# Performance work log

Measured on AMD Instinct MI355X. Metric: run time of the kernel, lower is better.

Reference implementation:

```python
import jax, jax.numpy as jnp
import numpy as np

FEATURE_MAPS = [8, 4, 2, 1]
BOXES_PER_LOC = [4, 6, 6, 4]
IMAGE_SIZE = 128
DECODED_SIZE = 64
Z_WHAT = 64
CHANNELS = [64, 256, 128, 64, 32, 16, 3]  # conv-transpose pyramid 1x1 -> 64x64
BATCH = 4
EMPTY_CONST = -1000.0
N_LOC = sum(f * f for f in FEATURE_MAPS)            # 85
N_BOX = sum(f * f * b for f, b in zip(FEATURE_MAPS, BOXES_PER_LOC))  # 380


def _recon_indices():
    # Decoder.reconstruction_indices: expand per-location latents to per-box.
    idx, last = [], 0
    for fm, bpl in zip(FEATURE_MAPS, BOXES_PER_LOC):
        for i in range(fm * fm):
            idx.append(np.full(bpl, last + i, dtype=np.int32))
        last += fm * fm
    return np.concatenate(idx)


def setup_inputs() -> dict:
    key = jax.random.key(0)
    ks = jax.random.split(key, 16)
    inp = {
        'z_what': jax.random.normal(ks[0], (BATCH, N_LOC, Z_WHAT), jnp.float32),
        'z_where': jax.random.uniform(ks[1], (BATCH, N_BOX, 4), jnp.float32),
        'z_present': jax.random.randint(ks[2], (BATCH, N_BOX, 1), 0, 2).astype(jnp.int32),
        'z_depth': jax.random.normal(ks[3], (BATCH, N_LOC, 1), jnp.float32),
    }
    for i, (cin, cout) in enumerate(zip(CHANNELS[:-1], CHANNELS[1:])):
        inp[f'w{i}'] = jax.random.normal(ks[4 + i], (2, 2, cin, cout), jnp.float32) / np.sqrt(4.0 * cin)
        inp[f'b{i}'] = jnp.zeros((cout,), jnp.float32)
    return inp


def _what_decoder(z_flat, params):
    # (N, Z) -> (N, 3, 64, 64): stack of stride-2 kernel-2 conv transposes.
    x = z_flat[:, :, None, None]
    n = len(params)
    for i, (w, b) in enumerate(params):
        x = jax.lax.conv_transpose(x, w, strides=(2, 2), padding='VALID',
                                   dimension_numbers=('NCHW', 'HWIO', 'NCHW'))
        x = x + b[None, :, None, None]
        x = jax.nn.sigmoid(x) if i == n - 1 else jax.nn.relu(x)
    return x


def _sample_bilinear(img, px, py):
    # img (3, D, D); px/py (S,) pixel coords along cols/rows; zero outside.
    D = DECODED_SIZE
    x0 = jnp.floor(px)
    y0 = jnp.floor(py)
    wx = px - x0
    wy = py - y0

    def gather(yi, xi):
        vy = (yi >= 0) & (yi <= D - 1)
        vx = (xi >= 0) & (xi <= D - 1)
        yc = jnp.clip(yi.astype(jnp.int32), 0, D - 1)
        xc = jnp.clip(xi.astype(jnp.int32), 0, D - 1)
        vals = img[:, yc[:, None], xc[None, :]]  # (3, S, S)
        return vals * (vy[:, None] & vx[None, :]).astype(img.dtype)

    g00 = gather(y0, x0)
    g01 = gather(y0, x0 + 1)
    g10 = gather(y0 + 1, x0)
    g11 = gather(y0 + 1, x0 + 1)
    wyc = wy[None, :, None]
    wxc = wx[None, None, :]
    return (g00 * (1 - wyc) * (1 - wxc) + g01 * (1 - wyc) * wxc
            + g10 * wyc * (1 - wxc) + g11 * wyc * wxc)


def _where_stn(imgs, z_where):
    # Paste each decoded glyph into an IMAGE_SIZE canvas at box (cx, cy, w, h).
    S, D = IMAGE_SIZE, DECODED_SIZE
    cx, cy, w, h = (z_where[:, i] for i in range(4))
    sx = jnp.maximum(w, 1e-5)
    sy = jnp.maximum(h, 1e-5)
    out = jnp.linspace(-1.0, 1.0, S)
    xin = (out[None, :] - (2 * cx - 1)[:, None]) / sx[:, None]  # (N, S)
    yin = (out[None, :] - (2 * cy - 1)[:, None]) / sy[:, None]
    px = (xin + 1) * (D - 1) / 2
    py = (yin + 1) * (D - 1) / 2
    return jax.vmap(_sample_bilinear)(imgs, px, py)  # (N, 3, S, S)


def reference(z_what, z_where, z_present, z_depth, w0, b0, w1, b1, w2, b2, w3, b3, w4, b4, w5, b5):
    params = [(w0, b0), (w1, b1), (w2, b2), (w3, b3), (w4, b4), (w5, b5)]
    idx = jnp.asarray(_recon_indices())
    zw = jnp.take(z_what, idx, axis=1)   # (B, N_BOX, Z)
    zd = jnp.take(z_depth, idx, axis=1)  # (B, N_BOX, 1)
    B = zw.shape[0]
    decoded = _what_decoder(zw.reshape(B * N_BOX, Z_WHAT), params)
    transformed = _where_stn(decoded, z_where.reshape(B * N_BOX, 4))
    recon = transformed.reshape(B, N_BOX, 3, IMAGE_SIZE, IMAGE_SIZE)
    depths = jnp.where(z_present[..., 0] == 1, zd[..., 0], EMPTY_CONST)  # (B, N_BOX)
    weights = jax.nn.softmax(depths, axis=1)
    return jnp.einsum('bn,bnchw->bchw', weights, recon)
```

## Files before the change

### kernel.cpp

```cpp
#include <hip/hip_runtime.h>
#include <hip/hip_bf16.h>

#define NBOX  380
#define NLOCS 85
#define NINST 340

__device__ __forceinline__ int loc_of_box(int n) {
    if (n < 256) return n >> 2;
    if (n < 352) return 64 + (n - 256) / 6;
    if (n < 376) return 80 + (n - 352) / 6;
    return 84;
}

__device__ __forceinline__ float f4e(const float4& v, int kk) {
    return (kk == 0) ? v.x : (kk == 1) ? v.y : (kk == 2) ? v.z : v.w;
}

__device__ void box_params_dev(int b, const float* __restrict__ zwhere,
    const int* __restrict__ zpresent, const float* __restrict__ zdepth,
    float* wgt, float* sxs, float* oxs, float* sys, float* oys,
    int* binst, int* rect, int* cidx, int* cnt, float* sm)
{
    float* sd  = sm;
    float* red = sm + 384;
    const int tid = threadIdx.x;

    if (tid < NBOX) {
        int loc = loc_of_box(tid);
        sd[tid] = (zpresent[b * NBOX + tid] == 1) ? zdepth[b * NLOCS + loc] : -1000.0f;
    }
    __syncthreads();

    float m = (tid < NBOX) ? sd[tid] : -1e30f;
    red[tid] = m; __syncthreads();
    for (int s = 256; s > 0; s >>= 1) {
        if (tid < s) red[tid] = fmaxf(red[tid], red[tid + s]);
        __syncthreads();
    }
    m = red[0]; __syncthreads();

    float sum = (tid < NBOX) ? expf(sd[tid] - m) : 0.f;
    red[tid] = sum; __syncthreads();
    for (int s = 256; s > 0; s >>= 1) {
        if (tid < s) red[tid] += red[tid + s];
        __syncthreads();
    }
    float inv = 1.0f / red[0];
    __syncthreads();

    if (tid < NBOX) {
        int g = b * NBOX + tid;
        float wv = expf(sd[tid] - m) * inv;
        wgt[g] = wv;
        float cx = zwhere[g * 4 + 0], cy = zwhere[g * 4 + 1];
        float w  = zwhere[g * 4 + 2], h  = zwhere[g * 4 + 3];
        float isx = 1.0f / fmaxf(w, 1e-5f);
        float isy = 1.0f / fmaxf(h, 1e-5f);
        float sxv = isx * (63.0f / 127.0f);
        float oxv = 31.5f * (1.0f - 2.0f * cx * isx);
        float syv = isy * (63.0f / 127.0f);
        float oyv = 31.5f * (1.0f - 2.0f * cy * isy);
        sxs[g] = sxv; oxs[g] = oxv; sys[g] = syv; oys[g] = oyv;
        binst[g] = b * NLOCS + loc_of_box(tid);
        int wlo = min(127, max(0, (int)floorf((-1.0f - oxv) / sxv)));
        int whi = max(0, min(127, (int)ceilf((64.0f - oxv) / sxv)));
        int hlo = min(127, max(0, (int)floorf((-1.0f - oyv) / syv)));
        int hhi = max(0, min(127, (int)ceilf((64.0f - oyv) / syv)));
        rect[g] = wlo | (whi << 8) | (hlo << 16) | (hhi << 24);
        sd[tid] = wv;
    }
    __syncthreads();

    if (tid < 64) {
        int base = 0;
        for (int c = 0; c < 6; ++c) {
            int n = c * 64 + tid;
            bool p = (n < NBOX) && (sd[n] > 0.0f);
            unsigned long long mask = __ballot(p);
            int pos = __popcll(mask & ((1ull << tid) - 1ull));
            if (p) cidx[b * NBOX + base + pos] = n;
            base += __popcll(mask);
        }
        if (tid == 0) cnt[b] = base;
    }
}

__global__ __launch_bounds__(512, 2) void decode_fused_k(
    const float* __restrict__ z_what,
    const float* __restrict__ W0, const float* __restrict__ B0,
    const float* __restrict__ W1, const float* __restrict__ B1,
    const float* __restrict__ W2, const float* __restrict__ B2,
    const float* __restrict__ W3, const float* __restrict__ B3,
    const float* __restrict__ W4, const float* __restrict__ B4,
    const float* __restrict__ W5, const float* __restrict__ B5,
    const float* __restrict__ z_where, const int* __restrict__ z_present,
    const float* __restrict__ z_depth,
    float* __restrict__ wgt, float* __restrict__ sxs, float* __restrict__ oxs,
    float* __restrict__ sys, float* __restrict__ oys, int* __restrict__ binst,
    int* __restrict__ rect, int* __restrict__ cidx, int* __restrict__ cnt,
    float* __restrict__ dec)
{
    __shared__ __align__(16) float sm[15360];

    const int bid = blockIdx.x;
    if (bid >= NINST) {
        box_params_dev(bid - NINST, z_where, z_present, z_depth,
                       wgt, sxs, oxs, sys, oys, binst, rect, cidx, cnt, sm);
        return;
    }
    const int loc = bid % 85;
    const int r2  = bid / 85;
    const int bp  = r2 & 1, s = r2 >> 1;
    const int inst0 = (2 * bp + 0) * 85 + loc;
    const int inst1 = (2 * bp + 1) * 85 + loc;

    const int tid = threadIdx.x;

    if (tid < 128) {
        int q = tid >> 6, l = tid & 63;
        sm[q * 7680 + 3584 + l] = z_what[(q ? inst1 : inst0) * 64 + l];
    }
    __syncthreads();

    {
        const int c0 = tid & 255, j0 = tid >> 8;
        const int ft = 3 - (2 * s + j0);
        const float* wp = W0 + (size_t)ft * 64 * 256 + c0;
        const float* x0 = sm + 3584;
        const float* x1 = sm + 7680 + 3584;
        float a0 = 0.f, a1 = 0.f;
        #pragma unroll 8
        for (int k = 0; k < 64; ++k) {
            float w = wp[k * 256];
            a0 = fmaf(x0[k], w, a0);
            a1 = fmaf(x1[k], w, a1);
        }
        float bb = B0[c0];
        sm[j0 * 256 + c0]        = fmaxf(a0 + bb, 0.f);
        sm[7680 + j0 * 256 + c0] = fmaxf(a1 + bb, 0.f);
    }
    __syncthreads();

    {
        const int c1 = tid & 127, t = tid >> 7;
        const int di = t >> 1, dj = t & 1, ft = 3 - t;
        const float* wp = W1 + (size_t)ft * 256 * 128 + c1;
        float aA0 = 0.f, aA1 = 0.f, aB0 = 0.f, aB1 = 0.f;
        #pragma unroll 4
        for (int kq = 0; kq < 64; ++kq) {
            int k0 = kq * 4;
            float4 vA0 = *(const float4*)&sm[0 * 256 + k0];
            float4 vA1 = *(const float4*)&sm[1 * 256 + k0];
            float4 vB0 = *(const float4*)&sm[7680 + 0 * 256 + k0];
            float4 vB1 = *(const float4*)&sm[7680 + 1 * 256 + k0];
            #pragma unroll
            for (int kk = 0; kk < 4; ++kk) {
                float w = wp[(k0 + kk) * 128];
                aA0 = fmaf(f4e(vA0, kk), w, aA0);
                aA1 = fmaf(f4e(vA1, kk), w, aA1);
                aB0 = fmaf(f4e(vB0, kk), w, aB0);
                aB1 = fmaf(f4e(vB1, kk), w, aB1);
            }
        }
        float bb = B1[c1];
        int o0 = (di * 4 + 0 + dj) * 128 + c1;
        int o1 = (di * 4 + 2 + dj) * 128 + c1;
        sm[512 + o0]        = fmaxf(aA0 + bb, 0.f);
        sm[512 + o1]        = fmaxf(aA1 + bb, 0.f);
        sm[7680 + 512 + o0] = fmaxf(aB0 + bb, 0.f);
        sm[7680 + 512 + o1] = fmaxf(aB1 + bb, 0.f);
    }
    __syncthreads();

    {
        const int c2 = tid & 63, x2 = tid >> 6;
        const int j = x2 >> 1, dj = x2 & 1;
        const float* wA = W2 + (size_t)(3 - dj) * 128 * 64 + c2;
        const float* wB = W2 + (size_t)(1 - dj) * 128 * 64 + c2;
        float acc[2][2][2];
        #pragma unroll
        for (int q = 0; q < 2; ++q)
            #pragma unroll
            for (int il = 0; il < 2; ++il) { acc[q][il][0] = 0.f; acc[q][il][1] = 0.f; }
        #pragma unroll 2
        for (int kq = 0; kq < 32; ++kq) {
            int k0 = kq * 4;
            float4 xr[2][2];
            #pragma unroll
            for (int q = 0; q < 2; ++q)
                #pragma unroll
                for (int il = 0; il < 2; ++il)
                    xr[q][il] = *(const float4*)&sm[q * 7680 + 512 + (il * 4 + j) * 128 + k0];
            #pragma unroll
            for (int kk = 0; kk < 4; ++kk) {
                float wa = wA[(k0 + kk) * 64], wb = wB[(k0 + kk) * 64];
                #pragma unroll
                for (int q = 0; q < 2; ++q)
                    #pragma unroll
                    for (int il = 0; il < 2; ++il) {
                        float e = f4e(xr[q][il], kk);
                        acc[q][il][0] = fmaf(e, wa, acc[q][il][0]);
                        acc[q][il][1] = fmaf(e, wb, acc[q][il][1]);
                    }
            }
        }
        float bb = B2[c2];
        #pragma unroll
        for (int q = 0; q < 2; ++q)
            #pragma unroll
            for (int il = 0; il < 2; ++il)
                #pragma unroll
                for (int di = 0; di < 2; ++di)
                    sm[q * 7680 + 1536 + ((2 * il + di) * 8 + x2) * 64 + c2] =
                        fmaxf(acc[q][il][di] + bb, 0.f);
    }
    __syncthreads();

    {
        const int c3 = tid & 31, x3 = tid >> 5;
        const int j = x3 >> 1, dj = x3 & 1;
        const float* wA = W3 + (size_t)(3 - dj) * 64 * 32 + c3;
        const float* wB = W3 + (size_t)(1 - dj) * 64 * 32 + c3;
        float acc[2][4][2];
        #pragma unroll
        for (int q = 0; q < 2; ++q)
            #pragma unroll
            for (int il = 0; il < 4; ++il) { acc[q][il][0] = 0.f; acc[q][il][1] = 0.f; }
        #pragma unroll 2
        for (int kq = 0; kq < 16; ++kq) {
            int k0 = kq * 4;
            float4 xr[2][4];
            #pragma unroll
            for (int q = 0; q < 2; ++q)
                #pragma unroll
                for (int il = 0; il < 4; ++il)
                    xr[q][il] = *(const float4*)&sm[q * 7680 + 1536 + (il * 8 + j) * 64 + k0];
            #pragma unroll
            for (int kk = 0; kk < 4; ++kk) {
                float wa = wA[(k0 + kk) * 32], wb = wB[(k0 + kk) * 32];
                #pragma unroll
                for (int q = 0; q < 2; ++q)
                    #pragma unroll
                    for (int il = 0; il < 4; ++il) {
                        float e = f4e(xr[q][il], kk);
                        acc[q][il][0] = fmaf(e, wa, acc[q][il][0]);
                        acc[q][il][1] = fmaf(e, wb, acc[q][il][1]);
                    }
            }
        }
        float bb = B3[c3];
        #pragma unroll
        for (int q = 0; q < 2; ++q)
            #pragma unroll
            for (int il = 0; il < 4; ++il)
                #pragma unroll
                for (int di = 0; di < 2; ++di)
                    sm[q * 7680 + 3584 + ((2 * il + di) * 16 + x3) * 32 + c3] =
                        fmaxf(acc[q][il][di] + bb, 0.f);
    }
    __syncthreads();

    const float b50 = B5[0], b51 = B5[1], b52 = B5[2];
    const int x5 = tid & 63, g5 = tid >> 6;
    const int dj5 = x5 & 1, di5 = g5 & 1;
    const int ft5 = 3 - (2 * di5 + dj5);
    float w5r[16][3];
    #pragma unroll
    for (int k = 0; k < 16; ++k) {
        w5r[k][0] = W5[(ft5 * 16 + k) * 3 + 0];
        w5r[k][1] = W5[(ft5 * 16 + k) * 3 + 1];
        w5r[k][2] = W5[(ft5 * 16 + k) * 3 + 2];
    }

    for (int c = 0; c < 4; ++c) {
        {
            const int c4 = tid & 15, x4 = tid >> 4;
            const int j = x4 >> 1, dj = x4 & 1;
            const float* wA = W4 + (size_t)(3 - dj) * 32 * 16 + c4;
            const float* wB = W4 + (size_t)(1 - dj) * 32 * 16 + c4;
            float acc[2][2][2];
            #pragma unroll
            for (int q = 0; q < 2; ++q)
                #pragma unroll
                for (int il = 0; il < 2; ++il) { acc[q][il][0] = 0.f; acc[q][il][1] = 0.f; }
            #pragma unroll
            for (int kq = 0; kq < 8; ++kq) {
                int k0 = kq * 4;
                float4 xr[2][2];
                #pragma unroll
                for (int q = 0; q < 2; ++q)
                    #pragma unroll
                    for (int il = 0; il < 2; ++il)
                        xr[q][il] = *(const float4*)
                            &sm[q * 7680 + 3584 + ((2 * c + il) * 16 + j) * 32 + k0];
                #pragma unroll
                for (int kk = 0; kk < 4; ++kk) {
                    float wa = wA[(k0 + kk) * 16], wb = wB[(k0 + kk) * 16];
                    #pragma unroll
                    for (int q = 0; q < 2; ++q)
                        #pragma unroll
                        for (int il = 0; il < 2; ++il) {
                            float e = f4e(xr[q][il], kk);
                            acc[q][il][0] = fmaf(e, wa, acc[q][il][0]);
                            acc[q][il][1] = fmaf(e, wb, acc[q][il][1]);
                        }
                }
            }
            float bb = B4[c4];
            #pragma unroll
            for (int q = 0; q < 2; ++q)
                #pragma unroll
                for (int il = 0; il < 2; ++il)
                    #pragma unroll
                    for (int di = 0; di < 2; ++di)
                        sm[q * 7680 + ((2 * il + di) * 32 + x4) * 17 + c4] =
                            fmaxf(acc[q][il][di] + bb, 0.f);
        }
        __syncthreads();
        {
            const int jl = x5 >> 1;
            const int lr = g5 >> 1;
            float a[2][3];
            #pragma unroll
            for (int q = 0; q < 2; ++q) { a[q][0] = b50; a[q][1] = b51; a[q][2] = b52; }
            #pragma unroll
            for (int k = 0; k < 16; ++k) {
                #pragma unroll
                for (int q = 0; q < 2; ++q) {
                    float xv = sm[q * 7680 + (lr * 32 + jl) * 17 + k];
                    a[q][0] = fmaf(xv, w5r[k][0], a[q][0]);
                    a[q][1] = fmaf(xv, w5r[k][1], a[q][1]);
                    a[q][2] = fmaf(xv, w5r[k][2], a[q][2]);
                }
            }
            int row = 32 * s + 8 * c + g5;
            #pragma unroll
            for (int q = 0; q < 2; ++q) {
                float v0 = 1.0f / (1.0f + expf(-a[q][0]));
                float v1 = 1.0f / (1.0f + expf(-a[q][1]));
                float v2 = 1.0f / (1.0f + expf(-a[q][2]));
                float* dp = dec + (size_t)(q ? inst1 : inst0) * 12288
                          + (size_t)(row * 64 + x5) * 3;
                dp[0] = v0; dp[1] = v1; dp[2] = v2;
            }
        }
        __syncthreads();
    }
}

__global__ __launch_bounds__(1024) void composite_k(
    const float* __restrict__ dec, const float* __restrict__ wgt,
    const float* __restrict__ sxs, const float* __restrict__ oxs,
    const float* __restrict__ sys, const float* __restrict__ oys,
    const int* __restrict__ binst, const int* __restrict__ rect,
    const int* __restrict__ cidx, const int* __restrict__ cnt,
    float* __restrict__ out)
{
    __shared__ float pls[8][128][3];

    int b = blockIdx.x >> 7, tile = blockIdx.x & 127;
    int tx0 = (tile & 7) << 4, ty0 = (tile >> 3) << 3;
    int s = threadIdx.x >> 7, px = threadIdx.x & 127;
    int lx = px & 15, ly = px >> 4;
    int w = tx0 + lx, h = ty0 + ly;

    int nb = cnt[b];
    int lo = (nb * s) >> 3, hi = (nb * (s + 1)) >> 3;

    float fw = (float)w, fh = (float)h;
    float a0 = 0.f, a1 = 0.f, a2 = 0.f;
    for (int q = lo; q < hi; ++q) {
        int n = cidx[b * NBOX + q];
        int rc = rect[b * NBOX + n];
        int wlo = rc & 255, whi = (rc >> 8) & 255;
        int hlo = (rc >> 16) & 255, hhi = (rc >> 24) & 255;
        if (whi < tx0 || wlo > tx0 + 15 || hhi < ty0 || hlo > ty0 + 7) continue;
        int g = b * NBOX + n;
        float wg = wgt[g];
        float pxx = fmaf(fw, sxs[g], oxs[g]);
        float pyy = fmaf(fh, sys[g], oys[g]);
        float x0 = floorf(pxx), y0 = floorf(pyy);
        if (x0 < -1.0f || x0 > 63.0f || y0 < -1.0f || y0 > 63.0f) continue;
        float wx = pxx - x0, wy = pyy - y0;
        int ix = (int)x0, iy = (int)y0;
        int x0c = max(ix, 0), x1c = min(ix + 1, 63);
        int y0c = max(iy, 0), y1c = min(iy + 1, 63);
        float m00 = (ix >= 0 && iy >= 0) ? 1.f : 0.f;
        float m01 = (ix + 1 <= 63 && iy >= 0) ? 1.f : 0.f;
        float m10 = (ix >= 0 && iy + 1 <= 63) ? 1.f : 0.f;
        float m11 = (ix + 1 <= 63 && iy + 1 <= 63) ? 1.f : 0.f;
        float w00 = (1.f - wy) * (1.f - wx) * m00;
        float w01 = (1.f - wy) * wx * m01;
        float w10 = wy * (1.f - wx) * m10;
        float w11 = wy * wx * m11;
        const float* img = dec + (size_t)binst[g] * 12288;
        int b00 = (y0c * 64 + x0c) * 3, b01 = (y0c * 64 + x1c) * 3;
        int b10 = (y1c * 64 + x0c) * 3, b11 = (y1c * 64 + x1c) * 3;
        a0 += wg * (w00 * img[b00]   + w01 * img[b01]   + w10 * img[b10]   + w11 * img[b11]);
        a1 += wg * (w00 * img[b00+1] + w01 * img[b01+1] + w10 * img[b10+1] + w11 * img[b11+1]);
        a2 += wg * (w00 * img[b00+2] + w01 * img[b01+2] + w10 * img[b10+2] + w11 * img[b11+2]);
    }
    pls[s][px][0] = a0; pls[s][px][1] = a1; pls[s][px][2] = a2;
    __syncthreads();

    if (threadIdx.x < 384) {
        int c = threadIdx.x >> 7, p2 = threadIdx.x & 127;
        float v = 0.f;
        #pragma unroll
        for (int t = 0; t < 8; ++t) v += pls[t][p2][c];
        int h2 = ty0 + (p2 >> 4), w2 = tx0 + (p2 & 15);
        out[((b * 3 + c) * 128 + h2) * 128 + w2] = v;
    }
}

extern "C" void kernel_launch(void* const* d_in, const int* in_sizes, int n_in,
                              void* d_out, int out_size, void* d_ws, size_t ws_size,
                              hipStream_t stream)
{
    const float* z_what    = (const float*)d_in[0];
    const float* z_where   = (const float*)d_in[1];
    const int*   z_present = (const int*)  d_in[2];
    const float* z_depth   = (const float*)d_in[3];

    char* ws = (char*)d_ws;
    float* dec = (float*)ws;
    float* P   = (float*)(ws + 16711680);
    float* wgt = P,        *sxs = P + 1520, *oxs = P + 2 * 1520;
    float* sys = P + 3 * 1520, *oys = P + 4 * 1520;
    int* binst = (int*)(P + 5 * 1520);
    int* rect  = binst + 1520;
    int* cidx  = binst + 2 * 1520;
    int* cnt   = binst + 3 * 1520;

    decode_fused_k<<<dim3(NINST + 4), dim3(512), 0, stream>>>(
        z_what,
        (const float*)d_in[4],  (const float*)d_in[5],
        (const float*)d_in[6],  (const float*)d_in[7],
        (const float*)d_in[8],  (const float*)d_in[9],
        (const float*)d_in[10], (const float*)d_in[11],
        (const float*)d_in[12], (const float*)d_in[13],
        (const float*)d_in[14], (const float*)d_in[15],
        z_where, z_present, z_depth,
        wgt, sxs, oxs, sys, oys, binst, rect, cidx, cnt,
        dec);

    composite_k<<<dim3(512), dim3(1024), 0, stream>>>(
        dec, wgt, sxs, oxs, sys, oys, binst, rect, cidx, cnt, (float*)d_out);
}
```

Measured before the change: 93.61 us.

## Restructure decoder conv stages to compute four output channels per thread with float4 weights

```diff
diff --git a/kernel.cpp b/kernel.cpp
--- a/kernel.cpp
+++ b/kernel.cpp
@@ -4,6 +4,7 @@
 #define NBOX  380
 #define NLOCS 85
 #define NINST 340
+#define SMB   7744
 
 __device__ __forceinline__ int loc_of_box(int n) {
     if (n < 256) return n >> 2;
@@ -100,7 +101,7 @@
     int* __restrict__ rect, int* __restrict__ cidx, int* __restrict__ cnt,
     float* __restrict__ dec)
 {
-    __shared__ __align__(16) float sm[15360];
+    __shared__ __align__(16) float sm[2 * SMB];
 
     const int bid = blockIdx.x;
     if (bid >= NINST) {
@@ -109,8 +110,8 @@
         return;
     }
     const int loc = bid % 85;
-    const int r2  = bid / 85;
-    const int bp  = r2 & 1, s = r2 >> 1;
+    const int r2g = bid / 85;
+    const int bp = r2g & 1, s = r2g >> 1;
     const int inst0 = (2 * bp + 0) * 85 + loc;
     const int inst1 = (2 * bp + 1) * 85 + loc;
 
@@ -118,7 +119,7 @@
 
     if (tid < 128) {
         int q = tid >> 6, l = tid & 63;
-        sm[q * 7680 + 3584 + l] = z_what[(q ? inst1 : inst0) * 64 + l];
+        sm[q * SMB + l] = z_what[(q ? inst1 : inst0) * 64 + l];
     }
     __syncthreads();
 
@@ -126,141 +127,132 @@
         const int c0 = tid & 255, j0 = tid >> 8;
         const int ft = 3 - (2 * s + j0);
         const float* wp = W0 + (size_t)ft * 64 * 256 + c0;
-        const float* x0 = sm + 3584;
-        const float* x1 = sm + 7680 + 3584;
-        float a0 = 0.f, a1 = 0.f;
-        #pragma unroll 8
-        for (int k = 0; k < 64; ++k) {
-            float w = wp[k * 256];
-            a0 = fmaf(x0[k], w, a0);
-            a1 = fmaf(x1[k], w, a1);
+        float aA = 0.f, aB = 0.f;
+        #pragma unroll 4
+        for (int kq = 0; kq < 16; ++kq) {
+            float4 xA = *(const float4*)&sm[kq * 4];
+            float4 xB = *(const float4*)&sm[SMB + kq * 4];
+            #pragma unroll
+            for (int kk = 0; kk < 4; ++kk) {
+                float w = wp[(kq * 4 + kk) * 256];
+                aA = fmaf(f4e(xA, kk), w, aA);
+                aB = fmaf(f4e(xB, kk), w, aB);
+            }
         }
         float bb = B0[c0];
-        sm[j0 * 256 + c0]        = fmaxf(a0 + bb, 0.f);
-        sm[7680 + j0 * 256 + c0] = fmaxf(a1 + bb, 0.f);
-    }
-    __syncthreads();
-
-    {
-        const int c1 = tid & 127, t = tid >> 7;
+        sm[64 + j0 * 256 + c0]       = fmaxf(aA + bb, 0.f);
+        sm[SMB + 64 + j0 * 256 + c0] = fmaxf(aB + bb, 0.f);
+    }
+    __syncthreads();
+
+    if (tid < 256) {
+        const int t = tid >> 6, co4 = (tid >> 1) & 31, j = tid & 1;
         const int di = t >> 1, dj = t & 1, ft = 3 - t;
-        const float* wp = W1 + (size_t)ft * 256 * 128 + c1;
-        float aA0 = 0.f, aA1 = 0.f, aB0 = 0.f, aB1 = 0.f;
+        const float* wp = W1 + (size_t)ft * 256 * 128 + co4 * 4;
+        float aA[4] = {0.f,0.f,0.f,0.f}, aB[4] = {0.f,0.f,0.f,0.f};
         #pragma unroll 4
         for (int kq = 0; kq < 64; ++kq) {
-            int k0 = kq * 4;
-            float4 vA0 = *(const float4*)&sm[0 * 256 + k0];
-            float4 vA1 = *(const float4*)&sm[1 * 256 + k0];
-            float4 vB0 = *(const float4*)&sm[7680 + 0 * 256 + k0];
-            float4 vB1 = *(const float4*)&sm[7680 + 1 * 256 + k0];
+            float4 xA = *(const float4*)&sm[64 + j * 256 + kq * 4];
+            float4 xB = *(const float4*)&sm[SMB + 64 + j * 256 + kq * 4];
             #pragma unroll
             for (int kk = 0; kk < 4; ++kk) {
-                float w = wp[(k0 + kk) * 128];
-                aA0 = fmaf(f4e(vA0, kk), w, aA0);
-                aA1 = fmaf(f4e(vA1, kk), w, aA1);
-                aB0 = fmaf(f4e(vB0, kk), w, aB0);
-                aB1 = fmaf(f4e(vB1, kk), w, aB1);
-            }
-        }
-        float bb = B1[c1];
-        int o0 = (di * 4 + 0 + dj) * 128 + c1;
-        int o1 = (di * 4 + 2 + dj) * 128 + c1;
-        sm[512 + o0]        = fmaxf(aA0 + bb, 0.f);
-        sm[512 + o1]        = fmaxf(aA1 + bb, 0.f);
-        sm[7680 + 512 + o0] = fmaxf(aB0 + bb, 0.f);
-        sm[7680 + 512 + o1] = fmaxf(aB1 + bb, 0.f);
+                float4 w4 = *(const float4*)&wp[(kq * 4 + kk) * 128];
+                float xa = f4e(xA, kk), xb = f4e(xB, kk);
+                aA[0] = fmaf(xa, w4.x, aA[0]); aA[1] = fmaf(xa, w4.y, aA[1]);
+                aA[2] = fmaf(xa, w4.z, aA[2]); aA[3] = fmaf(xa, w4.w, aA[3]);
+                aB[0] = fmaf(xb, w4.x, aB[0]); aB[1] = fmaf(xb, w4.y, aB[1]);
+                aB[2] = fmaf(xb, w4.z, aB[2]); aB[3] = fmaf(xb, w4.w, aB[3]);
+            }
+        }
+        float4 b4 = *(const float4*)&B1[co4 * 4];
+        int o = (di * 4 + 2 * j + dj) * 128 + co4 * 4;
+        *(float4*)&sm[576 + o] = make_float4(
+            fmaxf(aA[0] + b4.x, 0.f), fmaxf(aA[1] + b4.y, 0.f),
+            fmaxf(aA[2] + b4.z, 0.f), fmaxf(aA[3] + b4.w, 0.f));
+        *(float4*)&sm[SMB + 576 + o] = make_float4(
+            fmaxf(aB[0] + b4.x, 0.f), fmaxf(aB[1] + b4.y, 0.f),
+            fmaxf(aB[2] + b4.z, 0.f), fmaxf(aB[3] + b4.w, 0.f));
     }
     __syncthreads();
 
     {
-        const int c2 = tid & 63, x2 = tid >> 6;
-        const int j = x2 >> 1, dj = x2 & 1;
-        const float* wA = W2 + (size_t)(3 - dj) * 128 * 64 + c2;
-        const float* wB = W2 + (size_t)(1 - dj) * 128 * 64 + c2;
-        float acc[2][2][2];
-        #pragma unroll
-        for (int q = 0; q < 2; ++q)
-            #pragma unroll
-            for (int il = 0; il < 2; ++il) { acc[q][il][0] = 0.f; acc[q][il][1] = 0.f; }
-        #pragma unroll 2
+        const int orow = tid >> 7, ocol = (tid >> 4) & 7, co4 = tid & 15;
+        const int i = orow >> 1, di = orow & 1, j = ocol >> 1, dj = ocol & 1;
+        const int ft = 3 - (2 * di + dj);
+        const float* wp = W2 + (size_t)ft * 128 * 64 + co4 * 4;
+        float aA[4] = {0.f,0.f,0.f,0.f}, aB[4] = {0.f,0.f,0.f,0.f};
+        #pragma unroll 4
         for (int kq = 0; kq < 32; ++kq) {
-            int k0 = kq * 4;
-            float4 xr[2][2];
-            #pragma unroll
-            for (int q = 0; q < 2; ++q)
-                #pragma unroll
-                for (int il = 0; il < 2; ++il)
-                    xr[q][il] = *(const float4*)&sm[q * 7680 + 512 + (il * 4 + j) * 128 + k0];
+            float4 xA = *(const float4*)&sm[576 + (i * 4 + j) * 128 + kq * 4];
+            float4 xB = *(const float4*)&sm[SMB + 576 + (i * 4 + j) * 128 + kq * 4];
             #pragma unroll
             for (int kk = 0; kk < 4; ++kk) {
-                float wa = wA[(k0 + kk) * 64], wb = wB[(k0 + kk) * 64];
-                #pragma unroll
-                for (int q = 0; q < 2; ++q)
-                    #pragma unroll
-                    for (int il = 0; il < 2; ++il) {
-                        float e = f4e(xr[q][il], kk);
-                        acc[q][il][0] = fmaf(e, wa, acc[q][il][0]);
-                        acc[q][il][1] = fmaf(e, wb, acc[q][il][1]);
-                    }
-            }
-        }
-        float bb = B2[c2];
-        #pragma unroll
-        for (int q = 0; q < 2; ++q)
-            #pragma unroll
-            for (int il = 0; il < 2; ++il)
-                #pragma unroll
-                for (int di = 0; di < 2; ++di)
-                    sm[q * 7680 + 1536 + ((2 * il + di) * 8 + x2) * 64 + c2] =
-                        fmaxf(acc[q][il][di] + bb, 0.f);
+                float4 w4 = *(const float4*)&wp[(kq * 4 + kk) * 64];
+                float xa = f4e(xA, kk), xb = f4e(xB, kk);
+                aA[0] = fmaf(xa, w4.x, aA[0]); aA[1] = fmaf(xa, w4.y, aA[1]);
+                aA[2] = fmaf(xa, w4.z, aA[2]); aA[3] = fmaf(xa, w4.w, aA[3]);
+                aB[0] = fmaf(xb, w4.x, aB[0]); aB[1] = fmaf(xb, w4.y, aB[1]);
+                aB[2] = fmaf(xb, w4.z, aB[2]); aB[3] = fmaf(xb, w4.w, aB[3]);
+            }
+        }
+        float4 b4 = *(const float4*)&B2[co4 * 4];
+        int o = (orow * 8 + ocol) * 64 + co4 * 4;
+        *(float4*)&sm[1600 + o] = make_float4(
+            fmaxf(aA[0] + b4.x, 0.f), fmaxf(aA[1] + b4.y, 0.f),
+            fmaxf(aA[2] + b4.z, 0.f), fmaxf(aA[3] + b4.w, 0.f));
+        *(float4*)&sm[SMB + 1600 + o] = make_float4(
+            fmaxf(aB[0] + b4.x, 0.f), fmaxf(aB[1] + b4.y, 0.f),
+            fmaxf(aB[2] + b4.z, 0.f), fmaxf(aB[3] + b4.w, 0.f));
     }
     __syncthreads();
 
     {
-        const int c3 = tid & 31, x3 = tid >> 5;
-        const int j = x3 >> 1, dj = x3 & 1;
-        const float* wA = W3 + (size_t)(3 - dj) * 64 * 32 + c3;
-        const float* wB = W3 + (size_t)(1 - dj) * 64 * 32 + c3;
-        float acc[2][4][2];
-        #pragma unroll
-        for (int q = 0; q < 2; ++q)
-            #pragma unroll
-            for (int il = 0; il < 4; ++il) { acc[q][il][0] = 0.f; acc[q][il][1] = 0.f; }
+        const int orow = tid >> 6, ocol = (tid >> 3) & 7, co4 = tid & 7;
+        const int i = orow >> 1, di = orow & 1, dj = ocol & 1;
+        const int j1 = ocol >> 1, j2 = j1 + 4;
+        const int ft = 3 - (2 * di + dj);
+        const float* wp = W3 + (size_t)ft * 64 * 32 + co4 * 4;
+        float a1A[4] = {0.f,0.f,0.f,0.f}, a1B[4] = {0.f,0.f,0.f,0.f};
+        float a2A[4] = {0.f,0.f,0.f,0.f}, a2B[4] = {0.f,0.f,0.f,0.f};
         #pragma unroll 2
         for (int kq = 0; kq < 16; ++kq) {
-            int k0 = kq * 4;
-            float4 xr[2][4];
-            #pragma unroll
-            for (int q = 0; q < 2; ++q)
-                #pragma unroll
-                for (int il = 0; il < 4; ++il)
-                    xr[q][il] = *(const float4*)&sm[q * 7680 + 1536 + (il * 8 + j) * 64 + k0];
+            float4 x1A = *(const float4*)&sm[1600 + (i * 8 + j1) * 64 + kq * 4];
+            float4 x2A = *(const float4*)&sm[1600 + (i * 8 + j2) * 64 + kq * 4];
+            float4 x1B = *(const float4*)&sm[SMB + 1600 + (i * 8 + j1) * 64 + kq * 4];
+            float4 x2B = *(const float4*)&sm[SMB + 1600 + (i * 8 + j2) * 64 + kq * 4];
             #pragma unroll
             for (int kk = 0; kk < 4; ++kk) {
-                float wa = wA[(k0 + kk) * 32], wb = wB[(k0 + kk) * 32];
-                #pragma unroll
-                for (int q = 0; q < 2; ++q)
-                    #pragma unroll
-                    for (int il = 0; il < 4; ++il) {
-                        float e = f4e(xr[q][il], kk);
-                        acc[q][il][0] = fmaf(e, wa, acc[q][il][0]);
-                        acc[q][il][1] = fmaf(e, wb, acc[q][il][1]);
-                    }
-            }
-        }
-        float bb = B3[c3];
-        #pragma unroll
-        for (int q = 0; q < 2; ++q)
-            #pragma unroll
-            for (int il = 0; il < 4; ++il)
-                #pragma unroll
-                for (int di = 0; di < 2; ++di)
-                    sm[q * 7680 + 3584 + ((2 * il + di) * 16 + x3) * 32 + c3] =
-                        fmaxf(acc[q][il][di] + bb, 0.f);
-    }
-    __syncthreads();
-
-    const float b50 = B5[0], b51 = B5[1], b52 = B5[2];
+                float4 w4 = *(const float4*)&wp[(kq * 4 + kk) * 32];
+                float e1a = f4e(x1A, kk), e2a = f4e(x2A, kk);
+                float e1b = f4e(x1B, kk), e2b = f4e(x2B, kk);
+                a1A[0] = fmaf(e1a, w4.x, a1A[0]); a1A[1] = fmaf(e1a, w4.y, a1A[1]);
+                a1A[2] = fmaf(e1a, w4.z, a1A[2]); a1A[3] = fmaf(e1a, w4.w, a1A[3]);
+                a2A[0] = fmaf(e2a, w4.x, a2A[0]); a2A[1] = fmaf(e2a, w4.y, a2A[1]);
+                a2A[2] = fmaf(e2a, w4.z, a2A[2]); a2A[3] = fmaf(e2a, w4.w, a2A[3]);
+                a1B[0] = fmaf(e1b, w4.x, a1B[0]); a1B[1] = fmaf(e1b, w4.y, a1B[1]);
+                a1B[2] = fmaf(e1b, w4.z, a1B[2]); a1B[3] = fmaf(e1b, w4.w, a1B[3]);
+                a2B[0] = fmaf(e2b, w4.x, a2B[0]); a2B[1] = fmaf(e2b, w4.y, a2B[1]);
+                a2B[2] = fmaf(e2b, w4.z, a2B[2]); a2B[3] = fmaf(e2b, w4.w, a2B[3]);
+            }
+        }
+        float4 b4 = *(const float4*)&B3[co4 * 4];
+        int o1 = (orow * 16 + ocol) * 32 + co4 * 4;
+        int o2 = (orow * 16 + ocol + 8) * 32 + co4 * 4;
+        *(float4*)&sm[3648 + o1] = make_float4(
+            fmaxf(a1A[0] + b4.x, 0.f), fmaxf(a1A[1] + b4.y, 0.f),
+            fmaxf(a1A[2] + b4.z, 0.f), fmaxf(a1A[3] + b4.w, 0.f));
+        *(float4*)&sm[3648 + o2] = make_float4(
+            fmaxf(a2A[0] + b4.x, 0.f), fmaxf(a2A[1] + b4.y, 0.f),
+            fmaxf(a2A[2] + b4.z, 0.f), fmaxf(a2A[3] + b4.w, 0.f));
+        *(float4*)&sm[SMB + 3648 + o1] = make_float4(
+            fmaxf(a1B[0] + b4.x, 0.f), fmaxf(a1B[1] + b4.y, 0.f),
+            fmaxf(a1B[2] + b4.z, 0.f), fmaxf(a1B[3] + b4.w, 0.f));
+        *(float4*)&sm[SMB + 3648 + o2] = make_float4(
+            fmaxf(a2B[0] + b4.x, 0.f), fmaxf(a2B[1] + b4.y, 0.f),
+            fmaxf(a2B[2] + b4.z, 0.f), fmaxf(a2B[3] + b4.w, 0.f));
+    }
+    __syncthreads();
+
     const int x5 = tid & 63, g5 = tid >> 6;
     const int dj5 = x5 & 1, di5 = g5 & 1;
     const int ft5 = 3 - (2 * di5 + dj5);
@@ -271,78 +263,70 @@
         w5r[k][1] = W5[(ft5 * 16 + k) * 3 + 1];
         w5r[k][2] = W5[(ft5 * 16 + k) * 3 + 2];
     }
+    const float b50 = B5[0], b51 = B5[1], b52 = B5[2];
 
     for (int c = 0; c < 4; ++c) {
         {
-            const int c4 = tid & 15, x4 = tid >> 4;
-            const int j = x4 >> 1, dj = x4 & 1;
-            const float* wA = W4 + (size_t)(3 - dj) * 32 * 16 + c4;
-            const float* wB = W4 + (size_t)(1 - dj) * 32 * 16 + c4;
-            float acc[2][2][2];
-            #pragma unroll
-            for (int q = 0; q < 2; ++q)
-                #pragma unroll
-                for (int il = 0; il < 2; ++il) { acc[q][il][0] = 0.f; acc[q][il][1] = 0.f; }
+            const int ocol = tid >> 4, orow = (tid >> 2) & 3, co4 = tid & 3;
+            const int il3 = 2 * c + (orow >> 1), di = orow & 1;
+            const int j = ocol >> 1, dj = ocol & 1;
+            const int ft = 3 - (2 * di + dj);
+            const float* wp = W4 + (size_t)ft * 32 * 16 + co4 * 4;
+            float aA[4] = {0.f,0.f,0.f,0.f}, aB[4] = {0.f,0.f,0.f,0.f};
             #pragma unroll
             for (int kq = 0; kq < 8; ++kq) {
-                int k0 = kq * 4;
-                float4 xr[2][2];
-                #pragma unroll
-                for (int q = 0; q < 2; ++q)
-                    #pragma unroll
-                    for (int il = 0; il < 2; ++il)
-                        xr[q][il] = *(const float4*)
-                            &sm[q * 7680 + 3584 + ((2 * c + il) * 16 + j) * 32 + k0];
+                float4 xA = *(const float4*)&sm[3648 + (il3 * 16 + j) * 32 + kq * 4];
+                float4 xB = *(const float4*)&sm[SMB + 3648 + (il3 * 16 + j) * 32 + kq * 4];
                 #pragma unroll
                 for (int kk = 0; kk < 4; ++kk) {
-                    float wa = wA[(k0 + kk) * 16], wb = wB[(k0 + kk) * 16];
-                    #pragma unroll
-                    for (int q = 0; q < 2; ++q)
-                        #pragma unroll
-                        for (int il = 0; il < 2; ++il) {
-                            float e = f4e(xr[q][il], kk);
-                            acc[q][il][0] = fmaf(e, wa, acc[q][il][0]);
-                            acc[q][il][1] = fmaf(e, wb, acc[q][il][1]);
-                        }
+                    float4 w4 = *(const float4*)&wp[(kq * 4 + kk) * 16];
+                    float xa = f4e(xA, kk), xb = f4e(xB, kk);
+                    aA[0] = fmaf(xa, w4.x, aA[0]); aA[1] = fmaf(xa, w4.y, aA[1]);
+                    aA[2] = fmaf(xa, w4.z, aA[2]); aA[3] = fmaf(xa, w4.w, aA[3]);
+                    aB[0] = fmaf(xb, w4.x, aB[0]); aB[1] = fmaf(xb, w4.y, aB[1]);
+                    aB[2] = fmaf(xb, w4.z, aB[2]); aB[3] = fmaf(xb, w4.w, aB[3]);
                 }
             }
-            float bb = B4[c4];
-            #pragma unroll
-            for (int q = 0; q < 2; ++q)
-                #pragma unroll
-                for (int il = 0; il < 2; ++il)
-                    #pragma unroll
-                    for (int di = 0; di < 2; ++di)
-                        sm[q * 7680 + ((2 * il + di) * 32 + x4) * 17 + c4] =
-                            fmaxf(acc[q][il][di] + bb, 0.f);
+            float4 b4 = *(const float4*)&B4[co4 * 4];
+            int o = (orow * 32 + ocol) * 20 + co4 * 4;
+            *(float4*)&sm[o] = make_float4(
+                fmaxf(aA[0] + b4.x, 0.f), fmaxf(aA[1] + b4.y, 0.f),
+                fmaxf(aA[2] + b4.z, 0.f), fmaxf(aA[3] + b4.w, 0.f));
+            *(float4*)&sm[SMB + o] = make_float4(
+                fmaxf(aB[0] + b4.x, 0.f), fmaxf(aB[1] + b4.y, 0.f),
+                fmaxf(aB[2] + b4.z, 0.f), fmaxf(aB[3] + b4.w, 0.f));
         }
         __syncthreads();
         {
-            const int jl = x5 >> 1;
-            const int lr = g5 >> 1;
-            float a[2][3];
-            #pragma unroll
-            for (int q = 0; q < 2; ++q) { a[q][0] = b50; a[q][1] = b51; a[q][2] = b52; }
-            #pragma unroll
-            for (int k = 0; k < 16; ++k) {
+            const int j = x5 >> 1, lr = g5 >> 1;
+            const int base = (lr * 32 + j) * 20;
+            float aA0 = b50, aA1 = b51, aA2 = b52;
+            float aB0 = b50, aB1 = b51, aB2 = b52;
+            #pragma unroll
+            for (int kq = 0; kq < 4; ++kq) {
+                float4 xA = *(const float4*)&sm[base + kq * 4];
+                float4 xB = *(const float4*)&sm[SMB + base + kq * 4];
                 #pragma unroll
-                for (int q = 0; q < 2; ++q) {
-                    float xv = sm[q * 7680 + (lr * 32 + jl) * 17 + k];
-                    a[q][0] = fmaf(xv, w5r[k][0], a[q][0]);
-                    a[q][1] = fmaf(xv, w5r[k][1], a[q][1]);
-                    a[q][2] = fmaf(xv, w5r[k][2], a[q][2]);
+                for (int kk = 0; kk < 4; ++kk) {
+                    int k = kq * 4 + kk;
+                    float xa = f4e(xA, kk), xb = f4e(xB, kk);
+                    aA0 = fmaf(xa, w5r[k][0], aA0);
+                    aA1 = fmaf(xa, w5r[k][1], aA1);
+                    aA2 = fmaf(xa, w5r[k][2], aA2);
+                    aB0 = fmaf(xb, w5r[k][0], aB0);
+                    aB1 = fmaf(xb, w5r[k][1], aB1);
+                    aB2 = fmaf(xb, w5r[k][2], aB2);
                 }
             }
             int row = 32 * s + 8 * c + g5;
-            #pragma unroll
-            for (int q = 0; q < 2; ++q) {
-                float v0 = 1.0f / (1.0f + expf(-a[q][0]));
-                float v1 = 1.0f / (1.0f + expf(-a[q][1]));
-                float v2 = 1.0f / (1.0f + expf(-a[q][2]));
-                float* dp = dec + (size_t)(q ? inst1 : inst0) * 12288
-                          + (size_t)(row * 64 + x5) * 3;
-                dp[0] = v0; dp[1] = v1; dp[2] = v2;
-            }
+            float* dpA = dec + (size_t)inst0 * 12288 + (size_t)(row * 64 + x5) * 3;
+            float* dpB = dec + (size_t)inst1 * 12288 + (size_t)(row * 64 + x5) * 3;
+            dpA[0] = 1.0f / (1.0f + expf(-aA0));
+            dpA[1] = 1.0f / (1.0f + expf(-aA1));
+            dpA[2] = 1.0f / (1.0f + expf(-aA2));
+            dpB[0] = 1.0f / (1.0f + expf(-aB0));
+            dpB[1] = 1.0f / (1.0f + expf(-aB1));
+            dpB[2] = 1.0f / (1.0f + expf(-aB2));
         }
         __syncthreads();
     }
```

Result: slower. 129.0 us (+37.8%).
